# Optimization experiments

Measured on AMD Instinct MI355X. Metric: run time of the kernel, lower is better.

Reference implementation:

```python
import jax, jax.numpy as jnp
import numpy as np

EPS = 1e-5
NUM_GROUPS = 32


def setup_inputs() -> dict:
    key = jax.random.key(0)
    ks = jax.random.split(key, 4)
    b, c, h, w = 8, 512, 32, 32
    x = jax.random.normal(ks[0], (b, c, h, w), dtype=jnp.float32)
    gn_weight = jnp.ones((c,), dtype=jnp.float32)
    gn_bias = jnp.zeros((c,), dtype=jnp.float32)
    qkv_w = jax.random.normal(ks[1], (3 * c, c), dtype=jnp.float32) * (1.0 / np.sqrt(c))
    qkv_b = jnp.zeros((3 * c,), dtype=jnp.float32)
    proj_w = jax.random.normal(ks[2], (c, c), dtype=jnp.float32) * (1.0 / np.sqrt(c))
    proj_b = jnp.zeros((c,), dtype=jnp.float32)
    return {"x": x, "gn_weight": gn_weight, "gn_bias": gn_bias,
            "qkv_w": qkv_w, "qkv_b": qkv_b, "proj_w": proj_w, "proj_b": proj_b}


def _group_norm(x, weight, bias):
    b, c, h, w = x.shape
    xg = x.reshape(b, NUM_GROUPS, c // NUM_GROUPS, h, w)
    mean = xg.mean(axis=(2, 3, 4), keepdims=True)
    var = xg.var(axis=(2, 3, 4), keepdims=True)
    xn = ((xg - mean) * jax.lax.rsqrt(var + EPS)).reshape(b, c, h, w)
    return xn * weight[None, :, None, None] + bias[None, :, None, None]


def reference(x, gn_weight, gn_bias, qkv_w, qkv_b, proj_w, proj_b):
    b, c, h, w = x.shape
    scale = c ** (-0.5)
    xn = _group_norm(x, gn_weight, gn_bias)
    # 1x1 conv == per-pixel matmul over channels
    qkv = jnp.einsum('bchw,oc->bohw', xn, qkv_w) + qkv_b[None, :, None, None]
    q, k, v = jnp.split(qkv.reshape(b, 3 * c, h * w), 3, axis=1)  # each [b, c, N]
    attn = jax.nn.softmax(jnp.einsum('bci,bcj->bij', q, k) * scale, axis=-1)
    out = jnp.einsum('bij,bcj->bci', attn, v).reshape(b, c, h, w)
    proj = jnp.einsum('bchw,oc->bohw', out, proj_w) + proj_b[None, :, None, None]
    return x + proj
```

## Files before the change

### kernel.cpp

```cpp
#include <hip/hip_runtime.h>
#include <cmath>

constexpr int Bsz = 8, Cch = 512, NPIX = 1024;
constexpr int NG = 32, CPG = 16;

typedef __attribute__((ext_vector_type(4))) float f32x4;
typedef __attribute__((ext_vector_type(8))) short s16x8;

#define GLOBAL_AS __attribute__((address_space(1)))
#define LDS_AS __attribute__((address_space(3)))

__device__ inline short f2bf(float f) {
  union { float f; unsigned u; } c = {f};
  unsigned r = (c.u + 0x7fffu + ((c.u >> 16) & 1u)) >> 16;
  return (short)r;
}

__device__ inline float wave_reduce_sum(float v) {
#pragma unroll
  for (int off = 32; off > 0; off >>= 1) v += __shfl_xor(v, off, 64);
  return v;
}
__device__ inline float wave_reduce_max(float v) {
#pragma unroll
  for (int off = 32; off > 0; off >>= 1) v = fmaxf(v, __shfl_xor(v, off, 64));
  return v;
}

__global__ __launch_bounds__(256) void cvt_kernel(const float* __restrict__ in1,
                                                  short* __restrict__ out1, int n1,
                                                  const float* __restrict__ in2,
                                                  short* __restrict__ out2, int n2) {
  const int i = (blockIdx.x * 256 + threadIdx.x) * 4;
  const float* in = in1;
  short* out = out1;
  int j = i;
  if (i >= n1) { in = in2; out = out2; j = i - n1; }
  if (j + 3 < (i >= n1 ? n2 : n1)) {
    float4 v = *(const float4*)(in + j);
    short o[4] = {f2bf(v.x), f2bf(v.y), f2bf(v.z), f2bf(v.w)};
    *(uint2*)(out + j) = *(const uint2*)o;
  }
}

__global__ __launch_bounds__(256) void gn_kernel(
    const float* __restrict__ x, const float* __restrict__ w,
    const float* __restrict__ bb, short* __restrict__ xnt) {
  __shared__ float sm[8];
  const int bg = blockIdx.x, b = bg >> 5, g = bg & 31;
  const float* xp = x + ((size_t)(b * Cch + g * CPG)) * NPIX;
  float s = 0.f, ss = 0.f;
  for (int i = threadIdx.x * 4; i < CPG * NPIX; i += 1024) {
    float4 v = *(const float4*)(xp + i);
    s += v.x + v.y + v.z + v.w;
    ss += v.x * v.x + v.y * v.y + v.z * v.z + v.w * v.w;
  }
  s = wave_reduce_sum(s);
  ss = wave_reduce_sum(ss);
  const int wv = threadIdx.x >> 6;
  if ((threadIdx.x & 63) == 0) { sm[wv] = s; sm[4 + wv] = ss; }
  __syncthreads();
  const float tsum = sm[0] + sm[1] + sm[2] + sm[3];
  const float tsq = sm[4] + sm[5] + sm[6] + sm[7];
  const float inv_n = 1.0f / (CPG * NPIX);
  const float mean = tsum * inv_n;
  const float rstd = rsqrtf(tsq * inv_n - mean * mean + 1e-5f);
  float wc[CPG], bc[CPG];
#pragma unroll
  for (int c = 0; c < CPG; ++c) {
    wc[c] = w[g * CPG + c] * rstd;
    bc[c] = bb[g * CPG + c] - mean * wc[c];
  }
  for (int p = threadIdx.x; p < NPIX; p += 256) {
    short ov[CPG];
#pragma unroll
    for (int c = 0; c < CPG; ++c)
      ov[c] = f2bf(xp[(size_t)c * NPIX + p] * wc[c] + bc[c]);
    short* op = xnt + ((size_t)(b * NPIX + p)) * Cch + g * CPG;
    *(uint4*)op = *(const uint4*)&ov[0];
    *(uint4*)(op + 8) = *(const uint4*)&ov[8];
  }
}

template <int BM, int BN, int EPI>
__global__ __launch_bounds__(256) void mfma_gemm(
    const short* __restrict__ A, const short* __restrict__ B, int K, int lda,
    int ldb, long sA, long sB, const float* __restrict__ bias, float alpha,
    void* __restrict__ Cp, long sC, int ldc, void* __restrict__ C2p, long sC2,
    const float* __restrict__ resid, long sR) {
  constexpr int FM = BM / 32, FN = BN / 32;
  constexpr int NA = BM / 64, NB = BN / 64;
  __shared__ __align__(16) short Asl[BM * 32];
  __shared__ __align__(16) short Bsl[BN * 32];
  const int t = threadIdx.x;
  const int lane = t & 63, wave = t >> 6;
  const int bz = blockIdx.z;
  const int m0 = blockIdx.y * BM, n0 = blockIdx.x * BN;
  A += sA * bz;
  B += sB * bz;

  const short* ga[NA];
  const short* gb[NB];
  short* la[NA];
  short* lb[NB];
#pragma unroll
  for (int i = 0; i < NA; ++i) {
    const int s = i * 256 + t;
    const int row = ((s >> 6) * 16) + (s & 15);
    const int q = (s >> 4) & 3;
    ga[i] = A + (size_t)(m0 + row) * lda + q * 8;
    la[i] = Asl + s * 8;
  }
#pragma unroll
  for (int i = 0; i < NB; ++i) {
    const int s = i * 256 + t;
    const int row = ((s >> 6) * 16) + (s & 15);
    const int q = (s >> 4) & 3;
    gb[i] = B + (size_t)(n0 + row) * ldb + q * 8;
    lb[i] = Bsl + s * 8;
  }

  f32x4 acc[FM][FN] = {};
  const int wm = wave & 1, wn = wave >> 1;

  for (int k0 = 0; k0 < K; k0 += 32) {
#pragma unroll
    for (int i = 0; i < NA; ++i) {
      __builtin_amdgcn_global_load_lds((const GLOBAL_AS void*)ga[i],
                                       (LDS_AS void*)la[i], 16, 0, 0);
      ga[i] += 32;
    }
#pragma unroll
    for (int i = 0; i < NB; ++i) {
      __builtin_amdgcn_global_load_lds((const GLOBAL_AS void*)gb[i],
                                       (LDS_AS void*)lb[i], 16, 0, 0);
      gb[i] += 32;
    }
    __syncthreads();
    s16x8 af[FM], bf[FN];
#pragma unroll
    for (int i = 0; i < FM; ++i)
      af[i] = *(const s16x8*)(Asl + (wm * FM + i) * 512 + lane * 8);
#pragma unroll
    for (int i = 0; i < FN; ++i)
      bf[i] = *(const s16x8*)(Bsl + (wn * FN + i) * 512 + lane * 8);
#pragma unroll
    for (int im = 0; im < FM; ++im)
#pragma unroll
      for (int in = 0; in < FN; ++in)
        acc[im][in] = __builtin_amdgcn_mfma_f32_16x16x32_bf16(
            af[im], bf[in], acc[im][in], 0, 0, 0);
    __syncthreads();
  }

  const int quad = lane >> 4, nn = lane & 15;
#pragma unroll
  for (int im = 0; im < FM; ++im) {
#pragma unroll
    for (int in = 0; in < FN; ++in) {
      const int m = m0 + (wm * FM + im) * 16 + quad * 4;
      const int n = n0 + (wn * FN + in) * 16 + nn;
      if (EPI == 0) {
        if (m0 < 1024) {
          short* Cq = (short*)Cp + sC * bz;
          short o[4];
#pragma unroll
          for (int r = 0; r < 4; ++r) o[r] = f2bf(acc[im][in][r] + bias[m + r]);
          *(uint2*)(Cq + (size_t)n * ldc + m) = *(const uint2*)o;
        } else {
          short* Cv = (short*)C2p + sC2 * bz;
#pragma unroll
          for (int r = 0; r < 4; ++r)
            Cv[(size_t)(m - 1024 + r) * ldc + n] =
                f2bf(acc[im][in][r] + bias[m + r]);
        }
      } else if (EPI == 1) {
        float* Cf = (float*)Cp + sC * bz;
#pragma unroll
        for (int r = 0; r < 4; ++r)
          Cf[(size_t)(m + r) * ldc + n] = acc[im][in][r] * alpha;
      } else if (EPI == 2) {
        short* Cs = (short*)Cp + sC * bz;
#pragma unroll
        for (int r = 0; r < 4; ++r)
          Cs[(size_t)(m + r) * ldc + n] = f2bf(acc[im][in][r]);
      } else {
        float* Cf = (float*)Cp + sC * bz;
        const float* R = resid + sR * bz;
#pragma unroll
        for (int r = 0; r < 4; ++r)
          Cf[(size_t)(m + r) * ldc + n] =
              acc[im][in][r] + bias[m + r] + R[(size_t)(m + r) * ldc + n];
      }
    }
  }
}

__global__ __launch_bounds__(256) void softmax_kernel(const float* __restrict__ S,
                                                      short* __restrict__ P) {
  __shared__ float sm[8];
  const float* p = S + (size_t)blockIdx.x * 1024;
  const int t = threadIdx.x;
  float4 v = ((const float4*)p)[t];
  float mx = fmaxf(fmaxf(v.x, v.y), fmaxf(v.z, v.w));
  mx = wave_reduce_max(mx);
  if ((t & 63) == 0) sm[t >> 6] = mx;
  __syncthreads();
  mx = fmaxf(fmaxf(sm[0], sm[1]), fmaxf(sm[2], sm[3]));
  v.x = __expf(v.x - mx);
  v.y = __expf(v.y - mx);
  v.z = __expf(v.z - mx);
  v.w = __expf(v.w - mx);
  float s = v.x + v.y + v.z + v.w;
  s = wave_reduce_sum(s);
  if ((t & 63) == 0) sm[4 + (t >> 6)] = s;
  __syncthreads();
  const float inv = 1.0f / (sm[4] + sm[5] + sm[6] + sm[7]);
  short o[4] = {f2bf(v.x * inv), f2bf(v.y * inv), f2bf(v.z * inv),
                f2bf(v.w * inv)};
  *(uint2*)(P + (size_t)blockIdx.x * 1024 + t * 4) = *(const uint2*)o;
}

extern "C" void kernel_launch(void* const* d_in, const int* in_sizes, int n_in,
                              void* d_out, int out_size, void* d_ws,
                              size_t ws_size, hipStream_t stream) {
  const float* x = (const float*)d_in[0];
  const float* gnw = (const float*)d_in[1];
  const float* gnb = (const float*)d_in[2];
  const float* qkvw = (const float*)d_in[3];
  const float* qkvb = (const float*)d_in[4];
  const float* projw = (const float*)d_in[5];
  const float* projb = (const float*)d_in[6];
  float* out = (float*)d_out;

  char* ws = (char*)d_ws;
  short* xnt = (short*)ws;
  short* qkt = (short*)(ws + (8ull << 20));
  short* vbuf = (short*)(ws + (24ull << 20));
  float* Sbuf = (float*)(ws + (32ull << 20));
  short* Pbuf = (short*)(ws + (64ull << 20));
  short* Ot = (short*)(ws + (80ull << 20));
  short* wq = (short*)(ws + (88ull << 20));
  short* wp = (short*)(ws + (89ull << 20) + (512ull << 10));

  cvt_kernel<<<1024, 256, 0, stream>>>(qkvw, wq, 1536 * 512, projw, wp,
                                       512 * 512);

  gn_kernel<<<Bsz * NG, 256, 0, stream>>>(x, gnw, gnb, xnt);

  mfma_gemm<128, 128, 0><<<dim3(8, 12, Bsz), 256, 0, stream>>>(
      wq, xnt, 512, 512, 512, 0L, 1024L * 512, qkvb, 1.0f, qkt, 1024L * 1024,
      1024, vbuf, 512L * 1024, nullptr, 0L);

  const float scale = 1.0f / sqrtf(512.0f);
  mfma_gemm<128, 128, 1><<<dim3(8, 8, Bsz), 256, 0, stream>>>(
      qkt, qkt + 512, 512, 1024, 1024, 1024L * 1024, 1024L * 1024, nullptr,
      scale, Sbuf, 1024L * 1024, 1024, nullptr, 0L, nullptr, 0L);

  softmax_kernel<<<Bsz * 1024, 256, 0, stream>>>(Sbuf, Pbuf);

  mfma_gemm<128, 64, 2><<<dim3(8, 8, Bsz), 256, 0, stream>>>(
      Pbuf, vbuf, 1024, 1024, 1024, 1024L * 1024, 512L * 1024, nullptr, 1.0f,
      Ot, 1024L * 512, 512, nullptr, 0L, nullptr, 0L);

  mfma_gemm<64, 128, 3><<<dim3(8, 8, Bsz), 256, 0, stream>>>(
      wp, Ot, 512, 512, 512, 0L, 1024L * 512, projb, 1.0f, out, 512L * 1024,
      1024, nullptr, 0L, x, 512L * 1024);
}
```

Measured before the change: 205.3 us.

## Fuse prep kernels, deepen GEMM K-tile to 64, store scores in fp16

Three changes at once. The weight-conversion and group-norm kernels are merged into one launch, saving a launch and letting the two workloads overlap. The MFMA GEMM now loads 64-wide K slices per iteration, halving the number of barrier pairs at the cost of double the LDS per block. The attention score matrix is written and read as fp16 instead of fp32, halving the traffic of the score buffer between the QK GEMM and softmax, with some precision loss in the logits.

```diff
diff --git a/kernel.cpp b/kernel.cpp
--- a/kernel.cpp
+++ b/kernel.cpp
@@ -1,4 +1,5 @@
 #include <hip/hip_runtime.h>
+#include <hip/hip_fp16.h>
 #include <cmath>
 
 constexpr int Bsz = 8, Cch = 512, NPIX = 1024;
@@ -27,26 +28,25 @@
   return v;
 }
 
-__global__ __launch_bounds__(256) void cvt_kernel(const float* __restrict__ in1,
-                                                  short* __restrict__ out1, int n1,
-                                                  const float* __restrict__ in2,
-                                                  short* __restrict__ out2, int n2) {
-  const int i = (blockIdx.x * 256 + threadIdx.x) * 4;
-  const float* in = in1;
-  short* out = out1;
-  int j = i;
-  if (i >= n1) { in = in2; out = out2; j = i - n1; }
-  if (j + 3 < (i >= n1 ? n2 : n1)) {
-    float4 v = *(const float4*)(in + j);
-    short o[4] = {f2bf(v.x), f2bf(v.y), f2bf(v.z), f2bf(v.w)};
-    *(uint2*)(out + j) = *(const uint2*)o;
-  }
-}
-
-__global__ __launch_bounds__(256) void gn_kernel(
+__global__ __launch_bounds__(256) void prep_kernel(
     const float* __restrict__ x, const float* __restrict__ w,
-    const float* __restrict__ bb, short* __restrict__ xnt) {
+    const float* __restrict__ bb, short* __restrict__ xnt,
+    const float* __restrict__ in1, short* __restrict__ out1, int n1,
+    const float* __restrict__ in2, short* __restrict__ out2, int n2) {
   __shared__ float sm[8];
+  if (blockIdx.x >= 256) {
+    const int i = ((blockIdx.x - 256) * 256 + threadIdx.x) * 4;
+    const float* in = in1;
+    short* out = out1;
+    int j = i;
+    if (i >= n1) { in = in2; out = out2; j = i - n1; }
+    if (j + 3 < (i >= n1 ? n2 : n1)) {
+      float4 v = *(const float4*)(in + j);
+      short o[4] = {f2bf(v.x), f2bf(v.y), f2bf(v.z), f2bf(v.w)};
+      *(uint2*)(out + j) = *(const uint2*)o;
+    }
+    return;
+  }
   const int bg = blockIdx.x, b = bg >> 5, g = bg & 31;
   const float* xp = x + ((size_t)(b * Cch + g * CPG)) * NPIX;
   float s = 0.f, ss = 0.f;
@@ -89,9 +89,9 @@
     void* __restrict__ Cp, long sC, int ldc, void* __restrict__ C2p, long sC2,
     const float* __restrict__ resid, long sR) {
   constexpr int FM = BM / 32, FN = BN / 32;
-  constexpr int NA = BM / 64, NB = BN / 64;
-  __shared__ __align__(16) short Asl[BM * 32];
-  __shared__ __align__(16) short Bsl[BN * 32];
+  constexpr int NA = BM / 32, NB = BN / 32;
+  __shared__ __align__(16) short Asl[BM * 64];
+  __shared__ __align__(16) short Bsl[BN * 64];
   const int t = threadIdx.x;
   const int lane = t & 63, wave = t >> 6;
   const int bz = blockIdx.z;
@@ -105,51 +105,54 @@
   short* lb[NB];
 #pragma unroll
   for (int i = 0; i < NA; ++i) {
-    const int s = i * 256 + t;
-    const int row = ((s >> 6) * 16) + (s & 15);
-    const int q = (s >> 4) & 3;
-    ga[i] = A + (size_t)(m0 + row) * lda + q * 8;
-    la[i] = Asl + s * 8;
+    const int c = i * 256 + t;
+    const int row = ((c >> 7) << 4) + (c & 15);
+    const int koff = ((c >> 6) & 1) * 32 + ((c >> 4) & 3) * 8;
+    ga[i] = A + (size_t)(m0 + row) * lda + koff;
+    la[i] = Asl + c * 8;
   }
 #pragma unroll
   for (int i = 0; i < NB; ++i) {
-    const int s = i * 256 + t;
-    const int row = ((s >> 6) * 16) + (s & 15);
-    const int q = (s >> 4) & 3;
-    gb[i] = B + (size_t)(n0 + row) * ldb + q * 8;
-    lb[i] = Bsl + s * 8;
+    const int c = i * 256 + t;
+    const int row = ((c >> 7) << 4) + (c & 15);
+    const int koff = ((c >> 6) & 1) * 32 + ((c >> 4) & 3) * 8;
+    gb[i] = B + (size_t)(n0 + row) * ldb + koff;
+    lb[i] = Bsl + c * 8;
   }
 
   f32x4 acc[FM][FN] = {};
   const int wm = wave & 1, wn = wave >> 1;
 
-  for (int k0 = 0; k0 < K; k0 += 32) {
+  for (int k0 = 0; k0 < K; k0 += 64) {
 #pragma unroll
     for (int i = 0; i < NA; ++i) {
       __builtin_amdgcn_global_load_lds((const GLOBAL_AS void*)ga[i],
                                        (LDS_AS void*)la[i], 16, 0, 0);
-      ga[i] += 32;
+      ga[i] += 64;
     }
 #pragma unroll
     for (int i = 0; i < NB; ++i) {
       __builtin_amdgcn_global_load_lds((const GLOBAL_AS void*)gb[i],
                                        (LDS_AS void*)lb[i], 16, 0, 0);
-      gb[i] += 32;
+      gb[i] += 64;
     }
     __syncthreads();
-    s16x8 af[FM], bf[FN];
-#pragma unroll
-    for (int i = 0; i < FM; ++i)
-      af[i] = *(const s16x8*)(Asl + (wm * FM + i) * 512 + lane * 8);
-#pragma unroll
-    for (int i = 0; i < FN; ++i)
-      bf[i] = *(const s16x8*)(Bsl + (wn * FN + i) * 512 + lane * 8);
-#pragma unroll
-    for (int im = 0; im < FM; ++im)
-#pragma unroll
-      for (int in = 0; in < FN; ++in)
-        acc[im][in] = __builtin_amdgcn_mfma_f32_16x16x32_bf16(
-            af[im], bf[in], acc[im][in], 0, 0, 0);
+#pragma unroll
+    for (int p = 0; p < 2; ++p) {
+      s16x8 af[FM], bf[FN];
+#pragma unroll
+      for (int i = 0; i < FM; ++i)
+        af[i] = *(const s16x8*)(Asl + (wm * FM + i) * 1024 + p * 512 + lane * 8);
+#pragma unroll
+      for (int i = 0; i < FN; ++i)
+        bf[i] = *(const s16x8*)(Bsl + (wn * FN + i) * 1024 + p * 512 + lane * 8);
+#pragma unroll
+      for (int im = 0; im < FM; ++im)
+#pragma unroll
+        for (int in = 0; in < FN; ++in)
+          acc[im][in] = __builtin_amdgcn_mfma_f32_16x16x32_bf16(
+              af[im], bf[in], acc[im][in], 0, 0, 0);
+    }
     __syncthreads();
   }
 
@@ -175,10 +178,10 @@
                 f2bf(acc[im][in][r] + bias[m + r]);
         }
       } else if (EPI == 1) {
-        float* Cf = (float*)Cp + sC * bz;
+        __half* Ch = (__half*)Cp + sC * bz;
 #pragma unroll
         for (int r = 0; r < 4; ++r)
-          Cf[(size_t)(m + r) * ldc + n] = acc[im][in][r] * alpha;
+          Ch[(size_t)(m + r) * ldc + n] = __float2half(acc[im][in][r] * alpha);
       } else if (EPI == 2) {
         short* Cs = (short*)Cp + sC * bz;
 #pragma unroll
@@ -196,12 +199,15 @@
   }
 }
 
-__global__ __launch_bounds__(256) void softmax_kernel(const float* __restrict__ S,
+__global__ __launch_bounds__(256) void softmax_kernel(const __half* __restrict__ S,
                                                       short* __restrict__ P) {
   __shared__ float sm[8];
-  const float* p = S + (size_t)blockIdx.x * 1024;
+  const __half* p = S + (size_t)blockIdx.x * 1024;
   const int t = threadIdx.x;
-  float4 v = ((const float4*)p)[t];
+  uint2 raw = ((const uint2*)p)[t];
+  __half2 h0 = *(const __half2*)&raw.x, h1 = *(const __half2*)&raw.y;
+  float2 f0 = __half22float2(h0), f1 = __half22float2(h1);
+  float4 v = {f0.x, f0.y, f1.x, f1.y};
   float mx = fmaxf(fmaxf(v.x, v.y), fmaxf(v.z, v.w));
   mx = wave_reduce_max(mx);
   if ((t & 63) == 0) sm[t >> 6] = mx;
@@ -237,16 +243,14 @@
   short* xnt = (short*)ws;
   short* qkt = (short*)(ws + (8ull << 20));
   short* vbuf = (short*)(ws + (24ull << 20));
-  float* Sbuf = (float*)(ws + (32ull << 20));
+  __half* Sbuf = (__half*)(ws + (32ull << 20));
   short* Pbuf = (short*)(ws + (64ull << 20));
   short* Ot = (short*)(ws + (80ull << 20));
   short* wq = (short*)(ws + (88ull << 20));
   short* wp = (short*)(ws + (89ull << 20) + (512ull << 10));
 
-  cvt_kernel<<<1024, 256, 0, stream>>>(qkvw, wq, 1536 * 512, projw, wp,
-                                       512 * 512);
-
-  gn_kernel<<<Bsz * NG, 256, 0, stream>>>(x, gnw, gnb, xnt);
+  prep_kernel<<<1280, 256, 0, stream>>>(x, gnw, gnb, xnt, qkvw, wq, 1536 * 512,
+                                        projw, wp, 512 * 512);
 
   mfma_gemm<128, 128, 0><<<dim3(8, 12, Bsz), 256, 0, stream>>>(
       wq, xnt, 512, 512, 512, 0L, 1024L * 512, qkvb, 1.0f, qkt, 1024L * 1024,
```

After: 205.3 us. No clear change (+0.0%).
